# Performance work log

Measured on AMD Instinct MI355X. Metric: run time of the kernel, lower is better.

The kernel has to match this reference:

```python
import jax, jax.numpy as jnp
import numpy as np

# FlowNetC correlation config (matches init_kwargs)
PAD = 20          # pad_size
KERNEL = 1        # kernel_size (kernel_radius = 0)
MAX_DISP = 20     # max_displacement
STRIDE1 = 1       # output stride
STRIDE2 = 2       # displacement stride
RAD = MAX_DISP // STRIDE2   # neighborhood_grid_radius = 10 -> 21x21 = 441 displacements


def setup_inputs() -> dict:
    key = jax.random.key(0)
    k1, k2 = jax.random.split(key)
    B, C, H, W = 4, 256, 64, 96
    return {
        "input1": jax.random.normal(k1, (B, C, H, W), dtype=jnp.float32),
        "input2": jax.random.normal(k2, (B, C, H, W), dtype=jnp.float32),
    }


def reference(input1, input2):
    # input1, input2: [B, C, H, W]
    # Output: [B, (2*RAD+1)**2, H, W]  (pad_size == max_displacement, stride1 == 1,
    # kernel_size == 1 => output spatial size equals input spatial size).
    B, C, H, W = input1.shape
    p2 = jnp.pad(input2, ((0, 0), (0, 0), (PAD, PAD), (PAD, PAD)))
    norm = jnp.asarray(KERNEL * KERNEL * C, dtype=input1.dtype)
    outs = []
    # Fixed, small displacement grid (21x21): static slicing per displacement
    # avoids materializing a [441, B, C, H, W] intermediate.
    for dy in range(-RAD, RAD + 1):
        oy = PAD + dy * STRIDE2
        for dx in range(-RAD, RAD + 1):
            ox = PAD + dx * STRIDE2
            shifted = p2[:, :, oy:oy + H, ox:ox + W]        # [B, C, H, W]
            outs.append(jnp.sum(input1 * shifted, axis=1))  # [B, H, W]
    corr = jnp.stack(outs, axis=1) / norm                    # [B, 441, H, W]
    return corr
```

## Files before the change

kernel.cpp:

```cpp
#include <hip/hip_runtime.h>


typedef short bf16x8 __attribute__((ext_vector_type(8)));
typedef float f32x4  __attribute__((ext_vector_type(4)));

#define PLANE 24576
#define ST    40

__device__ __forceinline__ short f2bf(float f) {
    union { float f; unsigned u; } x; x.f = f;
    const unsigned u = x.u;
    return (short)((u + 0x7fffu + ((u >> 16) & 1u)) >> 16);
}

__global__ __launch_bounds__(512)
void corr_prepass(const float* __restrict__ in1, const float* __restrict__ in2,
                  short* __restrict__ dstA, short* __restrict__ dstB) {
    const int bid = blockIdx.x;
    const int sel = bid >> 8;
    const int r   = bid & 255;
    const int b   = r >> 6;
    const int yt  = (r >> 3) & 7;
    const int ct  = r & 7;
    const int c0 = ct * 32, y0 = yt * 8;
    const float* src = sel ? in2 : in1;
    short* dst = sel ? dstB : dstA;

    __shared__ __align__(16) short T[768 * ST];
    const int tid = threadIdx.x;

#pragma unroll
    for (int it = 0; it < 2; ++it) {
        const int d = it * 512 + tid;
        if (d < 768) {
            const int g = d / 192;
            const int f = d - g * 192;
            float4 v[8];
#pragma unroll
            for (int j = 0; j < 8; ++j) {
                const int c = c0 + g * 8 + j;
                v[j] = *(const float4*)(src + ((size_t)(b * 256 + c) * 64 + y0) * 96 + 4 * f);
            }
            bf16x8 w0, w1, w2, w3;
#pragma unroll
            for (int j = 0; j < 8; ++j) {
                w0[j] = f2bf(v[j].x); w1[j] = f2bf(v[j].y);
                w2[j] = f2bf(v[j].z); w3[j] = f2bf(v[j].w);
            }
            const int perm = ((g ^ (f & 3)) * 8);
            const int base = 4 * f * ST + perm;
            *(bf16x8*)&T[base]          = w0;
            *(bf16x8*)&T[base + ST]     = w1;
            *(bf16x8*)&T[base + 2*ST]   = w2;
            *(bf16x8*)&T[base + 3*ST]   = w3;
        }
    }
    __syncthreads();

#pragma unroll
    for (int it = 0; it < 6; ++it) {
        const int D  = it * 512 + tid;
        const int Rl = D >> 2, gp = D & 3;
        const int yy  = Rl / 96;
        const int rl  = Rl - yy * 96;
        const int par = rl / 48;
        const int col = rl - par * 48;
        const int x   = 2 * col + par;
        const int xx  = yy * 96 + x;
        const int perm = ((gp ^ ((xx >> 2) & 3)) * 8);
        const bf16x8 w = *(const bf16x8*)&T[xx * ST + perm];
        const size_t Rg = (size_t)(b * 64 + y0 + yy) * 96 + par * 48 + col;
        *(bf16x8*)(dst + Rg * 256 + c0 + gp * 8) = w;
    }
}

#define GLOAD(dst, ptr, imm) \
    asm volatile("global_load_dwordx4 %0, %1, off offset:%c2" \
                 : "=&v"(dst) : "v"(ptr), "n"(imm))

#define WAITV(N) \
    asm volatile("s_waitcnt vmcnt(" #N ")"); \
    __builtin_amdgcn_sched_barrier(0)

__global__ __launch_bounds__(512, 2)
void corr_mfma(const short* __restrict__ Ag, const short* __restrict__ Bg,
               float* __restrict__ out) {
    const int bhw = blockIdx.x;
    const int bid = ((bhw & 7) << 6) | (bhw >> 3);
    const int chunk = bid >> 6;
    const int b    = chunk >> 1;
    const int yhi  = chunk & 1;
    const int inner = bid & 63;
    const int par  = inner >> 5;
    const int y2   = (yhi << 5) | (inner & 31);
    const int by2  = b * 64 + y2;

    const int tid  = threadIdx.x;
    const int lane = tid & 63, slot = tid >> 6;
    const int n    = lane & 15, q = lane >> 4;

    __shared__ __align__(16) short Bsh[48 * 256];
    __shared__ __align__(16) float scr[8][1008];

    {
        const short* src = Bg + (size_t)by2 * PLANE + par * 48 * 256;
#pragma unroll
        for (int it = 0; it < 3; ++it) {
            const int j   = it * 512 + tid;
            const int row = j >> 5;
            const int ofs = (row * 256 + (j & 31) * 8) ^ ((row & 7) << 3);
            *(bf16x8*)&Bsh[ofs] = *(const bf16x8*)(src + j * 8);
        }
    }
    __syncthreads();

    const bool v0 = (n >= 10), v3 = (n < 10);
    const int r0 = v0 ? (n - 10) : 0;
    const int r1 = n + 6;
    const int r2 = n + 22;
    const int r3 = v3 ? (n + 38) : 0;

    float* const sc = scr[slot];

#pragma unroll
    for (int p = 0; p < 3; ++p) {
        const int dyp = p * 8 + slot;
        const int y   = y2 + 20 - 2 * dyp;
        const bool live = (dyp < 21) && (y >= 0) && (y < 64);
        if (!live) continue;

        f32x4 acc[9];
#pragma unroll
        for (int t2 = 0; t2 < 9; ++t2) acc[t2] = (f32x4)0.0f;

        const short* Ap  = Ag + ((size_t)(b * 64 + y) * 96 + par * 48) * 256
                         + n * 256 + q * 8;
        const short* ap0 = Ap;
        const short* ap1 = Ap + 4096;
        const short* ap2 = Ap + 8192;

        bf16x8 a0[3], a1[3], a2[3], a3[3];
        GLOAD(a0[0], ap0, 0);   GLOAD(a0[1], ap1, 0);   GLOAD(a0[2], ap2, 0);
        GLOAD(a1[0], ap0, 64);  GLOAD(a1[1], ap1, 64);  GLOAD(a1[2], ap2, 64);
        GLOAD(a2[0], ap0, 128); GLOAD(a2[1], ap1, 128); GLOAD(a2[2], ap2, 128);
        GLOAD(a3[0], ap0, 192); GLOAD(a3[1], ap1, 192); GLOAD(a3[2], ap2, 192);

#define STEP(ks, ab, NW, PF) { \
        WAITV(NW); \
        const int ko = (ks) * 32 + q * 8; \
        bf16x8 b0 = *(const bf16x8*)&Bsh[(r0 * 256 + ko) ^ ((r0 & 7) << 3)]; if (!v0) b0 = 0; \
        bf16x8 b1 = *(const bf16x8*)&Bsh[(r1 * 256 + ko) ^ ((r1 & 7) << 3)]; \
        bf16x8 b2 = *(const bf16x8*)&Bsh[(r2 * 256 + ko) ^ ((r2 & 7) << 3)]; \
        bf16x8 b3 = *(const bf16x8*)&Bsh[(r3 * 256 + ko) ^ ((r3 & 7) << 3)]; if (!v3) b3 = 0; \
        acc[0] = __builtin_amdgcn_mfma_f32_16x16x32_bf16(ab[0], b0, acc[0], 0, 0, 0); \
        acc[1] = __builtin_amdgcn_mfma_f32_16x16x32_bf16(ab[0], b1, acc[1], 0, 0, 0); \
        acc[2] = __builtin_amdgcn_mfma_f32_16x16x32_bf16(ab[0], b2, acc[2], 0, 0, 0); \
        acc[3] = __builtin_amdgcn_mfma_f32_16x16x32_bf16(ab[1], b1, acc[3], 0, 0, 0); \
        acc[4] = __builtin_amdgcn_mfma_f32_16x16x32_bf16(ab[1], b2, acc[4], 0, 0, 0); \
        acc[5] = __builtin_amdgcn_mfma_f32_16x16x32_bf16(ab[1], b3, acc[5], 0, 0, 0); \
        acc[6] = __builtin_amdgcn_mfma_f32_16x16x32_bf16(ab[2], b2, acc[6], 0, 0, 0); \
        acc[7] = __builtin_amdgcn_mfma_f32_16x16x32_bf16(ab[2], b3, acc[7], 0, 0, 0); \
        if (PF) { \
            GLOAD(ab[0], ap0, ((ks) + 4) * 64); \
            GLOAD(ab[1], ap1, ((ks) + 4) * 64); \
            GLOAD(ab[2], ap2, ((ks) + 4) * 64); \
        } \
    }

        STEP(0, a0, 9, 1) STEP(1, a1, 9, 1) STEP(2, a2, 9, 1) STEP(3, a3, 9, 1)
        STEP(4, a0, 9, 0) STEP(5, a1, 6, 0) STEP(6, a2, 3, 0) STEP(7, a3, 0, 0)
#undef STEP

        const int mb = q * 4;
#pragma unroll
        for (int t2 = 0; t2 < 9; ++t2) {
            const int Xi = (t2 < 3) ? 0 : (t2 < 6 ? 1 : 2);
            constexpr int UJ[9] = {0, 1, 2, 1, 2, 3, 2, 3, 4};
            const int ub = UJ[t2] * 16;
#pragma unroll
            for (int rr = 0; rr < 4; ++rr) {
                const int xe = Xi * 16 + mb + rr;
                const int k  = ub + n - xe;
                if ((unsigned)k < 21u)
                    sc[xe * 21 + k] = acc[t2][rr];
            }
        }

        const size_t obase = ((size_t)(b * 441 + dyp * 21) * 64 + y) * 96 + par;
        float vals[16];
#pragma unroll
        for (int it = 0; it < 16; ++it) {
            const int e = it * 64 + lane;
            vals[it] = (e < 1008) ? sc[(e % 48) * 21 + (e / 48)] : 0.0f;
        }
#pragma unroll
        for (int it = 0; it < 16; ++it) {
            const int e = it * 64 + lane;
            if (e < 1008) {
                const int k  = e / 48;
                const int xe = e - k * 48;
                out[obase + (size_t)k * 6144 + 2 * xe] = vals[it] * (1.0f / 256.0f);
            }
        }
    }
}

extern "C" void kernel_launch(void* const* d_in, const int* in_sizes, int n_in,
                              void* d_out, int out_size, void* d_ws, size_t ws_size,
                              hipStream_t stream) {
    const float* in1 = (const float*)d_in[0];
    const float* in2 = (const float*)d_in[1];
    float* out = (float*)d_out;

    short* Ag = (short*)d_ws;
    short* Bg = Ag + (size_t)256 * PLANE;

    corr_prepass<<<dim3(512), dim3(512), 0, stream>>>(in1, in2, Ag, Bg);
    corr_mfma<<<dim3(512), dim3(512), 0, stream>>>(Ag, Bg, out);
}
```

Measured before the change: 135.8 us.

## Prefetch next displacement row's A tiles during epilogue and interleave parity blocks

Issues the global loads for the next dy pass (row y-16) right after the current MFMA loop, so they overlap with the scatter and store epilogue instead of stalling at the start of the next pass. Wait counts are adjusted for the extra in-flight loads. The block-to-(par, y2) mapping also changes so that adjacent blocks alternate parity, which is meant to improve L2 locality. A memory clobber is added to the inline-asm load. In exchange, register pressure rises and the vmcnt bookkeeping becomes more fragile.

```diff
diff --git a/kernel.cpp b/kernel.cpp
--- a/kernel.cpp
+++ b/kernel.cpp
@@ -76,7 +76,7 @@
 
 #define GLOAD(dst, ptr, imm) \
     asm volatile("global_load_dwordx4 %0, %1, off offset:%c2" \
-                 : "=&v"(dst) : "v"(ptr), "n"(imm))
+                 : "=&v"(dst) : "v"(ptr), "n"(imm) : "memory")
 
 #define WAITV(N) \
     asm volatile("s_waitcnt vmcnt(" #N ")"); \
@@ -91,8 +91,8 @@
     const int b    = chunk >> 1;
     const int yhi  = chunk & 1;
     const int inner = bid & 63;
-    const int par  = inner >> 5;
-    const int y2   = (yhi << 5) | (inner & 31);
+    const int par  = inner & 1;
+    const int y2   = (yhi << 5) | (inner >> 1);
     const int by2  = b * 64 + y2;
 
     const int tid  = threadIdx.x;
@@ -122,28 +122,14 @@
 
     float* const sc = scr[slot];
 
-#pragma unroll
-    for (int p = 0; p < 3; ++p) {
-        const int dyp = p * 8 + slot;
-        const int y   = y2 + 20 - 2 * dyp;
-        const bool live = (dyp < 21) && (y >= 0) && (y < 64);
-        if (!live) continue;
-
-        f32x4 acc[9];
-#pragma unroll
-        for (int t2 = 0; t2 < 9; ++t2) acc[t2] = (f32x4)0.0f;
-
-        const short* Ap  = Ag + ((size_t)(b * 64 + y) * 96 + par * 48) * 256
-                         + n * 256 + q * 8;
-        const short* ap0 = Ap;
-        const short* ap1 = Ap + 4096;
-        const short* ap2 = Ap + 8192;
-
-        bf16x8 a0[3], a1[3], a2[3], a3[3];
-        GLOAD(a0[0], ap0, 0);   GLOAD(a0[1], ap1, 0);   GLOAD(a0[2], ap2, 0);
-        GLOAD(a1[0], ap0, 64);  GLOAD(a1[1], ap1, 64);  GLOAD(a1[2], ap2, 64);
-        GLOAD(a2[0], ap0, 128); GLOAD(a2[1], ap1, 128); GLOAD(a2[2], ap2, 128);
-        GLOAD(a3[0], ap0, 192); GLOAD(a3[1], ap1, 192); GLOAD(a3[2], ap2, 192);
+    bf16x8 a0[3], a1[3], a2[3], a3[3];
+    bool piped = false;
+
+#define LOAD12(P0, P1, P2) \
+        GLOAD(a0[0], P0, 0);   GLOAD(a0[1], P1, 0);   GLOAD(a0[2], P2, 0);   \
+        GLOAD(a1[0], P0, 64);  GLOAD(a1[1], P1, 64);  GLOAD(a1[2], P2, 64);  \
+        GLOAD(a2[0], P0, 128); GLOAD(a2[1], P1, 128); GLOAD(a2[2], P2, 128); \
+        GLOAD(a3[0], P0, 192); GLOAD(a3[1], P1, 192); GLOAD(a3[2], P2, 192);
 
 #define STEP(ks, ab, NW, PF) { \
         WAITV(NW); \
@@ -167,9 +153,46 @@
         } \
     }
 
-        STEP(0, a0, 9, 1) STEP(1, a1, 9, 1) STEP(2, a2, 9, 1) STEP(3, a3, 9, 1)
-        STEP(4, a0, 9, 0) STEP(5, a1, 6, 0) STEP(6, a2, 3, 0) STEP(7, a3, 0, 0)
-#undef STEP
+#pragma unroll
+    for (int p = 0; p < 3; ++p) {
+        const int dyp = p * 8 + slot;
+        const int y   = y2 + 20 - 2 * dyp;
+        const bool live = (dyp < 21) && (y >= 0) && (y < 64);
+        if (!live) { piped = false; continue; }
+
+        const short* Ap  = Ag + ((size_t)(b * 64 + y) * 96 + par * 48) * 256
+                         + n * 256 + q * 8;
+        const short* ap0 = Ap;
+        const short* ap1 = Ap + 4096;
+        const short* ap2 = Ap + 8192;
+
+        if (!piped) { LOAD12(ap0, ap1, ap2) }
+
+        f32x4 acc[9];
+#pragma unroll
+        for (int t2 = 0; t2 < 9; ++t2) acc[t2] = (f32x4)0.0f;
+
+        if (piped) {
+            STEP(0, a0, 25, 1) STEP(1, a1, 25, 1) STEP(2, a2, 25, 1) STEP(3, a3, 25, 1)
+            STEP(4, a0,  9, 0) STEP(5, a1,  6, 0) STEP(6, a2,  3, 0) STEP(7, a3,  0, 0)
+        } else {
+            STEP(0, a0,  9, 1) STEP(1, a1,  9, 1) STEP(2, a2,  9, 1) STEP(3, a3,  9, 1)
+            STEP(4, a0,  9, 0) STEP(5, a1,  6, 0) STEP(6, a2,  3, 0) STEP(7, a3,  0, 0)
+        }
+
+        {
+            const int yn = y - 16;
+            const bool live_n = (p < 2) && ((dyp + 8) < 21) && (yn >= 0);
+            if (live_n) {
+                const short* bp0 = ap0 - 393216;
+                const short* bp1 = ap1 - 393216;
+                const short* bp2 = ap2 - 393216;
+                LOAD12(bp0, bp1, bp2)
+                piped = true;
+            } else {
+                piped = false;
+            }
+        }
 
         const int mb = q * 4;
 #pragma unroll
@@ -203,6 +226,8 @@
             }
         }
     }
+#undef STEP
+#undef LOAD12
 }
 
 extern "C" void kernel_launch(void* const* d_in, const int* in_sizes, int n_in,
```

Result: no change. 134.2 us (-1.2%).
